# Kernel optimization log

Hardware: AMD Instinct MI355X
Metric: run time of the kernel (lower is better)

Reference implementation:

```python
import jax, jax.numpy as jnp
import numpy as np

NUM_GROUPS = 32
EPS = 1e-6


def group_norm(x, gamma, beta):
    # x: (B, C, H, W), 32 groups, eps=1e-6, affine
    B, C, H, W = x.shape
    xg = x.reshape(B, NUM_GROUPS, C // NUM_GROUPS, H, W)
    mean = xg.mean(axis=(2, 3, 4), keepdims=True)
    var = xg.var(axis=(2, 3, 4), keepdims=True)
    xn = ((xg - mean) * jax.lax.rsqrt(var + EPS)).reshape(B, C, H, W)
    return xn * gamma[None, :, None, None] + beta[None, :, None, None]


def conv1x1(x, w, b):
    # 1x1 conv == channel matmul. x: (B,C,H,W), w: (O,C), b: (O,)
    return jnp.einsum('bchw,oc->bohw', x, w) + b[None, :, None, None]


def setup_inputs() -> dict:
    key = jax.random.key(0)
    B, C, H, W = 16, 512, 32, 32
    ks = jax.random.split(key, 12)
    s = 1.0 / np.sqrt(C)
    return {
        'x': jax.random.normal(ks[0], (B, C, H, W), dtype=jnp.float32),
        'gn_gamma': jnp.ones((C,), dtype=jnp.float32),
        'gn_beta': jnp.zeros((C,), dtype=jnp.float32),
        'wq': jax.random.normal(ks[1], (C, C), dtype=jnp.float32) * s,
        'bq': jnp.zeros((C,), dtype=jnp.float32),
        'wk': jax.random.normal(ks[2], (C, C), dtype=jnp.float32) * s,
        'bk': jnp.zeros((C,), dtype=jnp.float32),
        'wv': jax.random.normal(ks[3], (C, C), dtype=jnp.float32) * s,
        'bv': jnp.zeros((C,), dtype=jnp.float32),
        'wp': jax.random.normal(ks[4], (C, C), dtype=jnp.float32) * s,
        'bp': jnp.zeros((C,), dtype=jnp.float32),
    }


def reference(x, gn_gamma, gn_beta, wq, bq, wk, bk, wv, bv, wp, bp):
    B, C, H, W = x.shape
    residual = x
    xn = group_norm(x, gn_gamma, gn_beta)
    q = conv1x1(xn, wq, bq).reshape(B, C, H * W)  # (B, C, HW)
    k = conv1x1(xn, wk, bk).reshape(B, C, H * W)
    v = conv1x1(xn, wv, bv).reshape(B, C, H * W)
    scale = C ** (-0.5)
    # energy[b,i,j] = q_i . k_j
    energy = jnp.einsum('bci,bcj->bij', q, k) * scale
    attn = jax.nn.softmax(energy, axis=-1)
    # out[b,c,i] = sum_j attn[b,i,j] * v[b,c,j]
    out = jnp.einsum('bij,bcj->bci', attn, v).reshape(B, C, H, W)
    out = conv1x1(out, wp, bp)
    return out + residual
```

## Files before the change

### kernel.cpp

```cpp
#include <hip/hip_runtime.h>
#include <hip/hip_bf16.h>

using bf16 = __hip_bfloat16;

typedef __attribute__((ext_vector_type(8))) __bf16 bf16x8;
typedef __attribute__((ext_vector_type(4))) float floatx4;

#define EPS 1e-6f

#define RAW_BARRIER()  asm volatile("s_barrier" ::: "memory")
#define WAIT_VM8()     asm volatile("s_waitcnt vmcnt(8)" ::: "memory")
#define WAIT_VM4()     asm volatile("s_waitcnt vmcnt(4)" ::: "memory")
#define WAIT_VM0()     asm volatile("s_waitcnt vmcnt(0)" ::: "memory")
#define PRIO1()        __builtin_amdgcn_s_setprio(1)
#define PRIO0()        __builtin_amdgcn_s_setprio(0)

__device__ __forceinline__ void load_lds16(const void* g, void* l) {
    __builtin_amdgcn_global_load_lds(
        (const __attribute__((address_space(1))) void*)g,
        (__attribute__((address_space(3))) void*)l, 16, 0, 0);
}

__device__ __forceinline__ void storeOut(float* p, float v) { *p = v; }
__device__ __forceinline__ void storeOut(bf16* p, float v) { *p = __float2bfloat16(v); }

#define MFMA16(a, b, c) __builtin_amdgcn_mfma_f32_16x16x32_bf16(a, b, c, 0, 0, 0)

template <int BIAS_MODE, int SCALE_EN, int RESID_EN, int EXP_MODE,
          int ROWDIV, int QKV, typename OutT>
__global__ __launch_bounds__(256, 2) void gemm2b(
    const bf16* __restrict__ A, long long aStride, int lda,
    const bf16* __restrict__ B, long long bStride, int ldb,
    OutT* __restrict__ D, long long dStride, int ldd,
    bf16* __restrict__ vout, long long vStride,
    const float* __restrict__ bias,
    const float* __restrict__ resid, long long rStride, int ldr,
    float* __restrict__ rowsum, int rsStride,
    int K, float scale, int tpb, int gx)
{
    constexpr int HB = 8192;
    extern __shared__ char smem[];

    const unsigned chunk = gridDim.x >> 3;
    const unsigned glob  = (blockIdx.x & 7) * chunk + (blockIdx.x >> 3);
    const unsigned z  = glob / (unsigned)tpb;
    const unsigned t  = glob % (unsigned)tpb;
    const int m0 = (int)(t / (unsigned)gx) << 7;
    const int n0 = (int)(t % (unsigned)gx) << 7;

    const int tid  = threadIdx.x;
    const int lane = tid & 63;
    const int wave = tid >> 6;
    const int wm   = wave >> 1;
    const int wn   = wave & 1;

    const bf16* Ab = A + (size_t)z * aStride + (size_t)m0 * lda;
    const bf16* Bb = B + (size_t)z * bStride + (size_t)n0 * ldb;

    floatx4 acc[4][4];
#pragma unroll
    for (int i = 0; i < 4; ++i)
#pragma unroll
        for (int j = 0; j < 4; ++j) acc[i][j] = (floatx4){0.f, 0.f, 0.f, 0.f};

    const int laneRow = lane & 15;
    const int laneKq  = lane >> 4;
    const int kqs16   = (laneKq ^ ((laneRow >> 1) & 3)) << 4;
    const int arow0   = wm * 64 + laneRow;
    const int brow0   = wn * 64 + laneRow;

    auto stage = [&](int kt, int h) {
        char* Adst = smem + ((kt & 1) * 2 + h) * HB;
        char* Bdst = smem + 4 * HB + ((kt & 1) * 2 + h) * HB;
        const int kb = (kt << 6) + (h << 5);
#pragma unroll
        for (int u = 0; u < 2; ++u) {
            const int idx = tid + u * 256;
            const int r  = idx >> 2;
            const int qs = (idx & 3) ^ ((idx >> 3) & 3);
            load_lds16(Ab + (size_t)r * lda + kb + qs * 8, Adst + idx * 16);
        }
#pragma unroll
        for (int u = 0; u < 2; ++u) {
            const int idx = tid + u * 256;
            const int r  = idx >> 2;
            const int qs = (idx & 3) ^ ((idx >> 3) & 3);
            load_lds16(Bb + (size_t)r * ldb + kb + qs * 8, Bdst + idx * 16);
        }
    };

    const int nt = K >> 6;
    stage(0, 0); stage(0, 1); stage(1, 0);

    for (int kt = 0; kt < nt; ++kt) {
        const char* Ablk = smem + (kt & 1) * 2 * HB;
        const char* Bblk = smem + 4 * HB + (kt & 1) * 2 * HB;
        const bool lastT = (kt == nt - 1);

        if (lastT) WAIT_VM4(); else WAIT_VM8();
        RAW_BARRIER();
        bf16x8 af[4], bfr[4];
#pragma unroll
        for (int im = 0; im < 4; ++im)
            af[im] = *(const bf16x8*)(Ablk + (arow0 + im * 16) * 64 + kqs16);
#pragma unroll
        for (int in = 0; in < 4; ++in)
            bfr[in] = *(const bf16x8*)(Bblk + (brow0 + in * 16) * 64 + kqs16);
        if (kt + 1 < nt) stage(kt + 1, 1);
        RAW_BARRIER();
        PRIO1();
#pragma unroll
        for (int im = 0; im < 4; ++im)
#pragma unroll
            for (int in = 0; in < 4; ++in)
                acc[im][in] = MFMA16(af[im], bfr[in], acc[im][in]);
        PRIO0();

        if (lastT) WAIT_VM0(); else WAIT_VM8();
        RAW_BARRIER();
#pragma unroll
        for (int im = 0; im < 4; ++im)
            af[im] = *(const bf16x8*)(Ablk + HB + (arow0 + im * 16) * 64 + kqs16);
#pragma unroll
        for (int in = 0; in < 4; ++in)
            bfr[in] = *(const bf16x8*)(Bblk + HB + (brow0 + in * 16) * 64 + kqs16);
        if (kt + 2 < nt) stage(kt + 2, 0);
        RAW_BARRIER();
        PRIO1();
#pragma unroll
        for (int im = 0; im < 4; ++im)
#pragma unroll
            for (int in = 0; in < 4; ++in)
                acc[im][in] = MFMA16(af[im], bfr[in], acc[im][in]);
        PRIO0();
    }

    const size_t dbase = (size_t)z * dStride;
#pragma unroll
    for (int im = 0; im < 4; ++im) {
        const int gmb = m0 + wm * 64 + im * 16 + (laneKq << 2);
        float ri[4];
        if (ROWDIV) {
#pragma unroll
            for (int r = 0; r < 4; ++r)
                ri[r] = 1.f / rowsum[(size_t)z * rsStride + gmb + r];
        }
        float rsum[4] = {0.f, 0.f, 0.f, 0.f};
#pragma unroll
        for (int in = 0; in < 4; ++in) {
            const int gn = n0 + wn * 64 + in * 16 + laneRow;
            float bn = 0.f;
            if (BIAS_MODE == 2) bn = bias[gn];
            if (QKV && n0 >= 1024) {
                union { bf16 h[4]; ushort4 u; } pk;
#pragma unroll
                for (int r = 0; r < 4; ++r)
                    pk.h[r] = __float2bfloat16(acc[im][in][r] + bn);
                *(ushort4*)(vout + (size_t)z * vStride +
                            (size_t)(gn - 1024) * 1024 + gmb) = pk.u;
            } else {
#pragma unroll
                for (int r = 0; r < 4; ++r) {
                    const int gm = gmb + r;
                    float v = acc[im][in][r];
                    if (SCALE_EN) v *= scale;
                    if (EXP_MODE) { v = __expf(v); rsum[r] += v; }
                    if (ROWDIV) v *= ri[r];
                    if (BIAS_MODE == 1) v += bias[gm];
                    if (BIAS_MODE == 2) v += bn;
                    if (RESID_EN)
                        v += resid[(size_t)z * rStride + (size_t)gm * ldr + gn];
                    storeOut(D + dbase + (size_t)gm * ldd + gn, v);
                }
            }
        }
        if (EXP_MODE) {
#pragma unroll
            for (int r = 0; r < 4; ++r) {
                float s = rsum[r];
                s += __shfl_xor(s, 1);
                s += __shfl_xor(s, 2);
                s += __shfl_xor(s, 4);
                s += __shfl_xor(s, 8);
                if (laneRow == 0)
                    atomicAdd(rowsum + (size_t)z * rsStride + gmb + r, s);
            }
        }
    }
}

__global__ __launch_bounds__(256) void gn_stats(const float* __restrict__ x,
                                                float* __restrict__ stats)
{
    const int bg = blockIdx.x;
    const float4* p = (const float4*)(x + (size_t)bg * 16384);
    float s = 0.f, ss = 0.f;
    for (int i = threadIdx.x; i < 4096; i += 256) {
        float4 v = p[i];
        s  += v.x + v.y + v.z + v.w;
        ss += v.x * v.x + v.y * v.y + v.z * v.z + v.w * v.w;
    }
#pragma unroll
    for (int off = 32; off; off >>= 1) {
        s  += __shfl_down(s, off);
        ss += __shfl_down(ss, off);
    }
    __shared__ float rs[4], rss[4];
    const int wv = threadIdx.x >> 6;
    if ((threadIdx.x & 63) == 0) { rs[wv] = s; rss[wv] = ss; }
    __syncthreads();
    if (threadIdx.x == 0) {
        float S  = rs[0] + rs[1] + rs[2] + rs[3];
        float SS = rss[0] + rss[1] + rss[2] + rss[3];
        float mean = S * (1.f / 16384.f);
        float var  = SS * (1.f / 16384.f) - mean * mean;
        stats[2 * bg]     = mean;
        stats[2 * bg + 1] = rsqrtf(var + EPS);
    }
}

__global__ __launch_bounds__(256) void gn_apply_t(const float* __restrict__ x,
                                                  const float* __restrict__ stats,
                                                  const float* __restrict__ gamma,
                                                  const float* __restrict__ beta,
                                                  bf16* __restrict__ xnT)
{
    __shared__ bf16 tile[32][36];
    const int b = blockIdx.z, c0 = blockIdx.y * 32, i0 = blockIdx.x * 32;
    {
        const int cc = threadIdx.x >> 3;
        const int i4 = (threadIdx.x & 7) << 2;
        const int c  = c0 + cc;
        const float mean = stats[2 * ((b << 5) + (c >> 4))];
        const float rstd = stats[2 * ((b << 5) + (c >> 4)) + 1];
        const float a  = gamma[c] * rstd;
        const float bb = beta[c] - mean * a;
        float4 v = *(const float4*)(x + (((size_t)(b * 512 + c)) << 10) + i0 + i4);
        tile[cc][i4 + 0] = __float2bfloat16(v.x * a + bb);
        tile[cc][i4 + 1] = __float2bfloat16(v.y * a + bb);
        tile[cc][i4 + 2] = __float2bfloat16(v.z * a + bb);
        tile[cc][i4 + 3] = __float2bfloat16(v.w * a + bb);
    }
    __syncthreads();
    {
        const int ii = threadIdx.x >> 3;
        const int c4 = (threadIdx.x & 7) << 2;
        union { bf16 h[4]; uint2 u; } pk;
        pk.h[0] = tile[c4 + 0][ii];
        pk.h[1] = tile[c4 + 1][ii];
        pk.h[2] = tile[c4 + 2][ii];
        pk.h[3] = tile[c4 + 3][ii];
        *((uint2*)(xnT + (((size_t)(b * 1024 + i0 + ii)) << 9) + c0 + c4)) = pk.u;
    }
}

__global__ __launch_bounds__(256) void prep(
    const float* __restrict__ wq, const float* __restrict__ wk,
    const float* __restrict__ wv, const float* __restrict__ wp,
    bf16* __restrict__ wqkvb, bf16* __restrict__ wpb,
    const float* __restrict__ bq, const float* __restrict__ bk,
    const float* __restrict__ bv, float* __restrict__ bqkv,
    float* __restrict__ rowsum)
{
    const int id = blockIdx.x;
    if (id < 1024) {
        const int w = id >> 8;
        const float* src = (w == 0) ? wq : (w == 1) ? wk : (w == 2) ? wv : wp;
        bf16* dst = (w < 3) ? (wqkvb + (size_t)w * 262144) : wpb;
        const int g = (id & 255) * 256 + threadIdx.x;
        float4 v = ((const float4*)src)[g];
        union { bf16 h[4]; uint2 u; } pk;
        pk.h[0] = __float2bfloat16(v.x);
        pk.h[1] = __float2bfloat16(v.y);
        pk.h[2] = __float2bfloat16(v.z);
        pk.h[3] = __float2bfloat16(v.w);
        ((uint2*)dst)[g] = pk.u;
    } else if (id == 1024) {
        for (int t = threadIdx.x; t < 1536; t += 256)
            bqkv[t] = (t < 512) ? bq[t] : (t < 1024) ? bk[t - 512] : bv[t - 1024];
    } else {
        float4 zero = {0.f, 0.f, 0.f, 0.f};
#pragma unroll
        for (int j = 0; j < 16; ++j)
            ((float4*)rowsum)[threadIdx.x + j * 256] = zero;
    }
}

extern "C" void kernel_launch(void* const* d_in, const int* in_sizes, int n_in,
                              void* d_out, int out_size, void* d_ws, size_t ws_size,
                              hipStream_t stream)
{
    const float* x     = (const float*)d_in[0];
    const float* gamma = (const float*)d_in[1];
    const float* beta  = (const float*)d_in[2];
    const float* wq    = (const float*)d_in[3];
    const float* bq    = (const float*)d_in[4];
    const float* wk    = (const float*)d_in[5];
    const float* bk    = (const float*)d_in[6];
    const float* wv    = (const float*)d_in[7];
    const float* bv    = (const float*)d_in[8];
    const float* wp    = (const float*)d_in[9];
    const float* bp    = (const float*)d_in[10];
    float* out = (float*)d_out;

    char* ws = (char*)d_ws;
    size_t off = 0;
    auto alloc = [&](size_t bytes) -> char* {
        char* p = ws + off;
        off += (bytes + 255) & ~(size_t)255;
        return p;
    };

    const long long S  = 1024, C = 512;
    const long long BS = S * C;
    const long long ES = S * S;

    float* stats  = (float*)alloc(512 * 2 * sizeof(float));
    float* bqkv   = (float*)alloc(1536 * sizeof(float));
    float* rowsum = (float*)alloc((size_t)16 * S * sizeof(float));
    bf16* wqkvb = (bf16*)alloc((size_t)3 * C * C * 2);
    bf16* wpb   = (bf16*)alloc((size_t)C * C * 2);
    bf16* xnT   = (bf16*)alloc((size_t)16 * BS * 2);
    bf16* qkT   = (bf16*)alloc((size_t)16 * ES * 2);
    bf16* vv    = (bf16*)alloc((size_t)16 * BS * 2);
    bf16* O2    = (bf16*)alloc((size_t)16 * BS * 2);

    int CB = 16;
    while (CB > 1 && off + (size_t)CB * ES * 2 + 1024 > ws_size) CB >>= 1;
    bf16* P = (bf16*)alloc((size_t)CB * ES * 2);

    hipFuncSetAttribute((const void*)gemm2b<2, 0, 0, 0, 0, 1, bf16>,
                        hipFuncAttributeMaxDynamicSharedMemorySize, 65536);
    hipFuncSetAttribute((const void*)gemm2b<0, 1, 0, 1, 0, 0, bf16>,
                        hipFuncAttributeMaxDynamicSharedMemorySize, 65536);
    hipFuncSetAttribute((const void*)gemm2b<0, 0, 0, 0, 1, 0, bf16>,
                        hipFuncAttributeMaxDynamicSharedMemorySize, 65536);
    hipFuncSetAttribute((const void*)gemm2b<1, 0, 1, 0, 0, 0, float>,
                        hipFuncAttributeMaxDynamicSharedMemorySize, 65536);

    prep<<<1026, 256, 0, stream>>>(wq, wk, wv, wp, wqkvb, wpb, bq, bk, bv,
                                   bqkv, rowsum);

    gn_stats<<<512, 256, 0, stream>>>(x, stats);
    gn_apply_t<<<dim3(32, 16, 16), 256, 0, stream>>>(x, stats, gamma, beta, xnT);

    gemm2b<2, 0, 0, 0, 0, 1, bf16><<<1536, 256, 65536, stream>>>(
        xnT, BS, 512, wqkvb, 0, 512, qkT, ES, 1024, vv, BS,
        bqkv, nullptr, 0, 0, nullptr, 0, 512, 1.f, 96, 12);

    const float scale = 0.044194173824159216f;
    for (int b0 = 0; b0 < 16; b0 += CB) {
        gemm2b<0, 1, 0, 1, 0, 0, bf16><<<CB * 64, 256, 65536, stream>>>(
            qkT + (size_t)b0 * ES, ES, 1024,
            qkT + (size_t)b0 * ES + 512, ES, 1024,
            P, ES, 1024, nullptr, 0,
            nullptr, nullptr, 0, 0, rowsum + (size_t)b0 * S, (int)S,
            512, scale, 64, 8);
        gemm2b<0, 0, 0, 0, 1, 0, bf16><<<CB * 32, 256, 65536, stream>>>(
            P, ES, 1024,
            vv + (size_t)b0 * BS, BS, 1024,
            O2 + (size_t)b0 * BS, BS, 512, nullptr, 0,
            nullptr, nullptr, 0, 0, rowsum + (size_t)b0 * S, (int)S,
            1024, 1.f, 32, 4);
    }

    gemm2b<1, 0, 1, 0, 0, 0, float><<<512, 256, 65536, stream>>>(
        wpb, 0, 512, O2, BS, 512, out, BS, 1024, nullptr, 0,
        bp, x, BS, 1024, nullptr, 0, 512, 1.f, 32, 8);
}
```

Measured before the change: 224.9 us.

## Fuse QK^T, exp and PV into a single flash-style attention kernel

Replaces the two-GEMM attention path, which wrote a full bf16 probability matrix P and accumulated row sums with atomics, with a fused kernel. Each block handles 64 query rows, keeps Q fragments in registers and streams K and V tiles through double-buffered LDS. Per tile it computes scores, exponentiates them without max subtraction, passes the bf16 probabilities through LDS and accumulates P·V, normalising by the row sum at the end. This removes the HBM traffic for P and the rowsum atomics. In exchange it launches only 256 blocks at one block per CU, uses large accumulator register pressure (32 floatx4), and skips the softmax max subtraction, which risks overflow for large scores.

```diff
diff --git a/kernel.cpp b/kernel.cpp
--- a/kernel.cpp
+++ b/kernel.cpp
@@ -9,6 +9,7 @@
 #define EPS 1e-6f
 
 #define RAW_BARRIER()  asm volatile("s_barrier" ::: "memory")
+#define WAIT_VM16()    asm volatile("s_waitcnt vmcnt(16)" ::: "memory")
 #define WAIT_VM8()     asm volatile("s_waitcnt vmcnt(8)" ::: "memory")
 #define WAIT_VM4()     asm volatile("s_waitcnt vmcnt(4)" ::: "memory")
 #define WAIT_VM0()     asm volatile("s_waitcnt vmcnt(0)" ::: "memory")
@@ -26,8 +27,7 @@
 
 #define MFMA16(a, b, c) __builtin_amdgcn_mfma_f32_16x16x32_bf16(a, b, c, 0, 0, 0)
 
-template <int BIAS_MODE, int SCALE_EN, int RESID_EN, int EXP_MODE,
-          int ROWDIV, int QKV, typename OutT>
+template <int BIAS_MODE, int RESID_EN, int QKV, typename OutT>
 __global__ __launch_bounds__(256, 2) void gemm2b(
     const bf16* __restrict__ A, long long aStride, int lda,
     const bf16* __restrict__ B, long long bStride, int ldb,
@@ -35,8 +35,7 @@
     bf16* __restrict__ vout, long long vStride,
     const float* __restrict__ bias,
     const float* __restrict__ resid, long long rStride, int ldr,
-    float* __restrict__ rowsum, int rsStride,
-    int K, float scale, int tpb, int gx)
+    int K, int tpb, int gx)
 {
     constexpr int HB = 8192;
     extern __shared__ char smem[];
@@ -139,13 +138,6 @@
 #pragma unroll
     for (int im = 0; im < 4; ++im) {
         const int gmb = m0 + wm * 64 + im * 16 + (laneKq << 2);
-        float ri[4];
-        if (ROWDIV) {
-#pragma unroll
-            for (int r = 0; r < 4; ++r)
-                ri[r] = 1.f / rowsum[(size_t)z * rsStride + gmb + r];
-        }
-        float rsum[4] = {0.f, 0.f, 0.f, 0.f};
 #pragma unroll
         for (int in = 0; in < 4; ++in) {
             const int gn = n0 + wn * 64 + in * 16 + laneRow;
@@ -163,9 +155,6 @@
                 for (int r = 0; r < 4; ++r) {
                     const int gm = gmb + r;
                     float v = acc[im][in][r];
-                    if (SCALE_EN) v *= scale;
-                    if (EXP_MODE) { v = __expf(v); rsum[r] += v; }
-                    if (ROWDIV) v *= ri[r];
                     if (BIAS_MODE == 1) v += bias[gm];
                     if (BIAS_MODE == 2) v += bn;
                     if (RESID_EN)
@@ -174,18 +163,132 @@
                 }
             }
         }
-        if (EXP_MODE) {
-#pragma unroll
-            for (int r = 0; r < 4; ++r) {
-                float s = rsum[r];
-                s += __shfl_xor(s, 1);
-                s += __shfl_xor(s, 2);
-                s += __shfl_xor(s, 4);
-                s += __shfl_xor(s, 8);
-                if (laneRow == 0)
-                    atomicAdd(rowsum + (size_t)z * rsStride + gmb + r, s);
-            }
-        }
+    }
+}
+
+__global__ __launch_bounds__(256, 1) void fattn(
+    const bf16* __restrict__ qkT,
+    const bf16* __restrict__ vv,
+    bf16* __restrict__ O2,
+    float scale)
+{
+    constexpr int KT = 32768;
+    extern __shared__ char smem[];
+    __shared__ __align__(16) char plds[4 * 1024];
+
+    const int bid  = blockIdx.x;
+    const int glob = (bid & 7) * 32 + (bid >> 3);
+    const int b    = glob >> 4;
+    const int i0   = (glob & 15) << 6;
+
+    const int tid     = threadIdx.x;
+    const int lane    = tid & 63;
+    const int wave    = tid >> 6;
+    const int laneRow = lane & 15;
+    const int laneKq  = lane >> 4;
+    const int kqs16   = (laneKq ^ ((laneRow >> 1) & 3)) << 4;
+
+    const bf16* Qb = qkT + (size_t)b * 1048576 + (size_t)(i0 + wave * 16) * 1024;
+    const bf16* Kb = qkT + (size_t)b * 1048576 + 512;
+    const bf16* Vb = vv + (size_t)b * 524288;
+
+    bf16x8 qf[16];
+#pragma unroll
+    for (int ks = 0; ks < 16; ++ks)
+        qf[ks] = *(const bf16x8*)(Qb + (size_t)laneRow * 1024 + ks * 32 + laneKq * 8);
+
+    floatx4 acc[32];
+#pragma unroll
+    for (int mf = 0; mf < 32; ++mf) acc[mf] = (floatx4){0.f, 0.f, 0.f, 0.f};
+    float rs = 0.f;
+
+    auto stageK = [&](int jt) {
+        char* dst = smem + (jt & 1) * KT;
+        const bf16* src = Kb + ((size_t)jt << 5) * 1024;
+#pragma unroll
+        for (int u = 0; u < 8; ++u) {
+            const int idx = tid + u * 256;
+            const int kk = idx >> 7;
+            const int j  = (idx >> 2) & 31;
+            const int p  = idx & 3;
+            load_lds16(src + (size_t)j * 1024 + kk * 32 + 8 * (p ^ ((j >> 1) & 3)),
+                       dst + idx * 16);
+        }
+    };
+    auto stageV = [&](int jt) {
+        char* dst = smem + 2 * KT + (jt & 1) * KT;
+        const bf16* src = Vb + (jt << 5);
+#pragma unroll
+        for (int u = 0; u < 8; ++u) {
+            const int idx = tid + u * 256;
+            const int c = idx >> 2;
+            const int p = idx & 3;
+            load_lds16(src + (size_t)c * 1024 + 8 * (p ^ ((c >> 1) & 3)),
+                       dst + idx * 16);
+        }
+    };
+
+    stageK(0); stageV(0); stageK(1); stageV(1);
+
+    char* pl = plds + wave * 1024 + laneRow * 64;
+    const int sw2 = ((laneRow >> 1) & 3) << 1;
+
+    for (int jt = 0; jt < 32; ++jt) {
+        if (jt == 31) WAIT_VM0(); else WAIT_VM16();
+        RAW_BARRIER();
+        const char* Kt = smem + (jt & 1) * KT;
+        const char* Vt = smem + 2 * KT + (jt & 1) * KT;
+
+        floatx4 s0 = (floatx4){0.f, 0.f, 0.f, 0.f};
+        floatx4 s1 = (floatx4){0.f, 0.f, 0.f, 0.f};
+#pragma unroll
+        for (int ks = 0; ks < 16; ++ks) {
+            bf16x8 kf0 = *(const bf16x8*)(Kt + ks * 2048 + laneRow * 64 + kqs16);
+            bf16x8 kf1 = *(const bf16x8*)(Kt + ks * 2048 + (laneRow + 16) * 64 + kqs16);
+            s0 = MFMA16(kf0, qf[ks], s0);
+            s1 = MFMA16(kf1, qf[ks], s1);
+        }
+
+        union { bf16 h[4]; unsigned long long u; } w0, w1;
+#pragma unroll
+        for (int r = 0; r < 4; ++r) {
+            float v0 = __expf(s0[r] * scale);
+            float v1 = __expf(s1[r] * scale);
+            rs += v0 + v1;
+            w0.h[r] = __float2bfloat16(v0);
+            w1.h[r] = __float2bfloat16(v1);
+        }
+        *(unsigned long long*)(pl + ((laneKq)     ^ sw2) * 8) = w0.u;
+        *(unsigned long long*)(pl + ((laneKq + 4) ^ sw2) * 8) = w1.u;
+        asm volatile("s_waitcnt lgkmcnt(0)" ::: "memory");
+        __builtin_amdgcn_sched_barrier(0);
+        bf16x8 pf = *(const bf16x8*)(pl + kqs16);
+
+        PRIO1();
+#pragma unroll
+        for (int mf = 0; mf < 32; ++mf) {
+            bf16x8 vf = *(const bf16x8*)(Vt + (laneRow + 16 * mf) * 64 + kqs16);
+            acc[mf] = MFMA16(vf, pf, acc[mf]);
+        }
+        PRIO0();
+
+        RAW_BARRIER();
+        if (jt + 2 < 32) { stageK(jt + 2); stageV(jt + 2); }
+    }
+
+    rs += __shfl_xor(rs, 16);
+    rs += __shfl_xor(rs, 32);
+    const float ri = 1.f / rs;
+
+    bf16* Ob = O2 + (size_t)b * 524288 +
+               (size_t)(i0 + wave * 16 + laneRow) * 512 + (laneKq << 2);
+#pragma unroll
+    for (int mf = 0; mf < 32; ++mf) {
+        union { bf16 h[4]; ushort4 u; } pk;
+#pragma unroll
+        for (int r = 0; r < 4; ++r)
+            pk.h[r] = __float2bfloat16(acc[mf][r] * ri);
+        *(ushort4*)(Ob + mf * 16) = pk.u;
     }
 }
 
@@ -259,8 +362,7 @@
     const float* __restrict__ wv, const float* __restrict__ wp,
     bf16* __restrict__ wqkvb, bf16* __restrict__ wpb,
     const float* __restrict__ bq, const float* __restrict__ bk,
-    const float* __restrict__ bv, float* __restrict__ bqkv,
-    float* __restrict__ rowsum)
+    const float* __restrict__ bv, float* __restrict__ bqkv)
 {
     const int id = blockIdx.x;
     if (id < 1024) {
@@ -275,14 +377,9 @@
         pk.h[2] = __float2bfloat16(v.z);
         pk.h[3] = __float2bfloat16(v.w);
         ((uint2*)dst)[g] = pk.u;
-    } else if (id == 1024) {
+    } else {
         for (int t = threadIdx.x; t < 1536; t += 256)
             bqkv[t] = (t < 512) ? bq[t] : (t < 1024) ? bk[t - 512] : bv[t - 1024];
-    } else {
-        float4 zero = {0.f, 0.f, 0.f, 0.f};
-#pragma unroll
-        for (int j = 0; j < 16; ++j)
-            ((float4*)rowsum)[threadIdx.x + j * 256] = zero;
     }
 }
 
@@ -317,7 +414,6 @@
 
     float* stats  = (float*)alloc(512 * 2 * sizeof(float));
     float* bqkv   = (float*)alloc(1536 * sizeof(float));
-    float* rowsum = (float*)alloc((size_t)16 * S * sizeof(float));
     bf16* wqkvb = (bf16*)alloc((size_t)3 * C * C * 2);
     bf16* wpb   = (bf16*)alloc((size_t)C * C * 2);
     bf16* xnT   = (bf16*)alloc((size_t)16 * BS * 2);
@@ -325,46 +421,26 @@
     bf16* vv    = (bf16*)alloc((size_t)16 * BS * 2);
     bf16* O2    = (bf16*)alloc((size_t)16 * BS * 2);
 
-    int CB = 16;
-    while (CB > 1 && off + (size_t)CB * ES * 2 + 1024 > ws_size) CB >>= 1;
-    bf16* P = (bf16*)alloc((size_t)CB * ES * 2);
-
-    hipFuncSetAttribute((const void*)gemm2b<2, 0, 0, 0, 0, 1, bf16>,
+    hipFuncSetAttribute((const void*)gemm2b<2, 0, 1, bf16>,
                         hipFuncAttributeMaxDynamicSharedMemorySize, 65536);
-    hipFuncSetAttribute((const void*)gemm2b<0, 1, 0, 1, 0, 0, bf16>,
+    hipFuncSetAttribute((const void*)gemm2b<1, 1, 0, float>,
                         hipFuncAttributeMaxDynamicSharedMemorySize, 65536);
-    hipFuncSetAttribute((const void*)gemm2b<0, 0, 0, 0, 1, 0, bf16>,
-                        hipFuncAttributeMaxDynamicSharedMemorySize, 65536);
-    hipFuncSetAttribute((const void*)gemm2b<1, 0, 1, 0, 0, 0, float>,
-                        hipFuncAttributeMaxDynamicSharedMemorySize, 65536);
-
-    prep<<<1026, 256, 0, stream>>>(wq, wk, wv, wp, wqkvb, wpb, bq, bk, bv,
-                                   bqkv, rowsum);
+    hipFuncSetAttribute((const void*)fattn,
+                        hipFuncAttributeMaxDynamicSharedMemorySize, 131072);
+
+    prep<<<1025, 256, 0, stream>>>(wq, wk, wv, wp, wqkvb, wpb, bq, bk, bv, bqkv);
 
     gn_stats<<<512, 256, 0, stream>>>(x, stats);
     gn_apply_t<<<dim3(32, 16, 16), 256, 0, stream>>>(x, stats, gamma, beta, xnT);
 
-    gemm2b<2, 0, 0, 0, 0, 1, bf16><<<1536, 256, 65536, stream>>>(
+    gemm2b<2, 0, 1, bf16><<<1536, 256, 65536, stream>>>(
         xnT, BS, 512, wqkvb, 0, 512, qkT, ES, 1024, vv, BS,
-        bqkv, nullptr, 0, 0, nullptr, 0, 512, 1.f, 96, 12);
+        bqkv, nullptr, 0, 0, 512, 96, 12);
 
     const float scale = 0.044194173824159216f;
-    for (int b0 = 0; b0 < 16; b0 += CB) {
-        gemm2b<0, 1, 0, 1, 0, 0, bf16><<<CB * 64, 256, 65536, stream>>>(
-            qkT + (size_t)b0 * ES, ES, 1024,
-            qkT + (size_t)b0 * ES + 512, ES, 1024,
-            P, ES, 1024, nullptr, 0,
-            nullptr, nullptr, 0, 0, rowsum + (size_t)b0 * S, (int)S,
-            512, scale, 64, 8);
-        gemm2b<0, 0, 0, 0, 1, 0, bf16><<<CB * 32, 256, 65536, stream>>>(
-            P, ES, 1024,
-            vv + (size_t)b0 * BS, BS, 1024,
-            O2 + (size_t)b0 * BS, BS, 512, nullptr, 0,
-            nullptr, nullptr, 0, 0, rowsum + (size_t)b0 * S, (int)S,
-            1024, 1.f, 32, 4);
-    }
-
-    gemm2b<1, 0, 1, 0, 0, 0, float><<<512, 256, 65536, stream>>>(
+    fattn<<<256, 256, 131072, stream>>>(qkT, vv, O2, scale);
+
+    gemm2b<1, 1, 0, float><<<512, 256, 65536, stream>>>(
         wpb, 0, 512, O2, BS, 512, out, BS, 1024, nullptr, 0,
-        bp, x, BS, 1024, nullptr, 0, 512, 1.f, 32, 8);
-}
+        bp, x, BS, 1024, 512, 32, 8);
+}
```

Measured after the change: 254.2 us. 1.13x slower.
